# Performance work log

Measured on AMD Instinct MI355X. Metric: run time of the kernel, lower is better.

## Reference

```python
import jax, jax.numpy as jnp
import numpy as np

QUALITY = 8
N_PART = 18000 * QUALITY ** 2  # 1,152,000
N_GRID = 128 * QUALITY         # 1024
DX = 1.0 / N_GRID
INV_DX = float(N_GRID)
DT = 1e-4 / QUALITY
P_VOL = (DX * 0.5) ** 2
P_MASS = P_VOL * 1.0
E_MOD, NU = 5000.0, 0.2
MU0 = E_MOD / (2.0 * (1.0 + NU))
LAM0 = E_MOD * NU / ((1.0 + NU) * (1.0 - 2.0 * NU))
OFF = jnp.array([[i, j] for i in range(3) for j in range(3)], dtype=jnp.int32)  # [9,2]


def setup_inputs() -> dict:
    key = jax.random.key(0)
    ks = jax.random.split(key, 6)
    x = 0.05 + 0.9 * jax.random.uniform(ks[0], (N_PART, 2), dtype=jnp.float32)
    v = jax.random.normal(ks[1], (N_PART, 2), dtype=jnp.float32)
    C = 0.1 * jax.random.normal(ks[2], (N_PART, 2, 2), dtype=jnp.float32)
    F = jnp.eye(2, dtype=jnp.float32) + 0.02 * jax.random.normal(ks[3], (N_PART, 2, 2), dtype=jnp.float32)
    material = jax.random.randint(ks[4], (N_PART,), 0, 3, dtype=jnp.int32)
    Jp = 0.5 + jax.random.uniform(ks[5], (N_PART,), dtype=jnp.float32)
    gravity = jnp.array([0.0, -1.0], dtype=jnp.float32)
    attractor_strength = jnp.array(1.0, dtype=jnp.float32)
    attractor_pos = jnp.array([0.5, 0.5], dtype=jnp.float32)
    return dict(x=x, v=v, C=C, F=F, Jp=Jp, gravity=gravity,
                attractor_strength=attractor_strength, attractor_pos=attractor_pos,
                material=material)


def _substep(x, v, C, F, Jp, gravity, attractor_strength, attractor_pos, material):
    I2 = jnp.eye(2, dtype=x.dtype)
    # ---- per-particle quadratic B-spline weights ----
    base = jnp.floor(x * INV_DX - 0.5).astype(jnp.int32)            # [P,2]
    fx = x * INV_DX - base.astype(x.dtype)                           # [P,2]
    w = jnp.stack([0.5 * (1.5 - fx) ** 2,
                   0.75 - (fx - 1.0) ** 2,
                   0.5 * (fx - 0.5) ** 2], axis=1)                   # [P,3,2]
    weight = w[:, OFF[:, 0], 0] * w[:, OFF[:, 1], 1]                 # [P,9]

    # ---- deformation update + elastoplastic stress ----
    F = jnp.einsum('pij,pjk->pik', I2 + DT * C, F)                   # [P,2,2]
    h = jnp.clip(jnp.exp(10.0 * (1.0 - Jp)), 0.1, 5.0)
    h = jnp.where(material == 1, 0.3, h)
    mu = jnp.where(material == 0, 0.0, MU0 * h)                      # [P]
    la = LAM0 * h
    U, sig, Vh = jnp.linalg.svd(F)                                   # sig [P,2]
    new_sig = jnp.where((material == 2)[:, None],
                        jnp.clip(sig, 1.0 - 2.5e-2, 1.0 + 4.5e-3), sig)
    Jp = Jp * jnp.prod(sig / new_sig, axis=1)
    J = jnp.prod(new_sig, axis=1)                                    # [P]
    F_fluid = jnp.sqrt(J)[:, None, None] * I2
    F_snow = jnp.einsum('pij,pj,pjk->pik', U, new_sig, Vh)
    F = jnp.where((material == 0)[:, None, None], F_fluid,
                  jnp.where((material == 2)[:, None, None], F_snow, F))
    R = jnp.einsum('pij,pjk->pik', U, Vh)                            # rotation U V^T
    stress = (2.0 * mu[:, None, None] *
              jnp.einsum('pij,pkj->pik', F - R, F) +
              (la * J * (J - 1.0))[:, None, None] * I2)
    stress = (-DT * P_VOL * 4.0 * INV_DX * INV_DX) * stress
    affine = stress + P_MASS * C                                     # [P,2,2]

    # ---- P2G scatter-add ----
    dpos = (OFF.astype(x.dtype)[None] - fx[:, None, :]) * DX         # [P,9,2]
    mom = weight[:, :, None] * (P_MASS * v[:, None, :] +
                                jnp.einsum('pab,pkb->pka', affine, dpos))
    gi = jnp.clip(base[:, None, 0] + OFF[None, :, 0], 0, N_GRID - 1)
    gj = jnp.clip(base[:, None, 1] + OFF[None, :, 1], 0, N_GRID - 1)
    idx = (gi * N_GRID + gj).reshape(-1)                              # [P*9]
    grid_v = jnp.zeros((N_GRID * N_GRID, 2), x.dtype).at[idx].add(mom.reshape(-1, 2))
    grid_m = jnp.zeros((N_GRID * N_GRID,), x.dtype).at[idx].add((weight * P_MASS).reshape(-1))

    # ---- grid update ----
    gv = grid_v.reshape(N_GRID, N_GRID, 2)
    gm = grid_m.reshape(N_GRID, N_GRID)
    mask = gm > 0
    gv = jnp.where(mask[..., None], gv / jnp.where(mask, gm, 1.0)[..., None], 0.0)
    gv = gv + DT * 30.0 * gravity                                    # broadcast [2]
    ii, jj = jnp.meshgrid(jnp.arange(N_GRID), jnp.arange(N_GRID), indexing='ij')
    coords = DX * jnp.stack([ii, jj], axis=-1).astype(x.dtype)        # [G,G,2]
    dist = attractor_pos - coords
    gv = gv + dist / (0.01 + jnp.linalg.norm(dist, axis=-1, keepdims=True)) \
              * attractor_strength * DT * 100.0
    gvx, gvy = gv[..., 0], gv[..., 1]
    gvx = jnp.where((ii < 3) & (gvx < 0), 0.0, gvx)
    gvx = jnp.where((ii > N_GRID - 3) & (gvx > 0), 0.0, gvx)
    gvy = jnp.where((jj < 3) & (gvy < 0), 0.0, gvy)
    gvy = jnp.where((jj > N_GRID - 3) & (gvy > 0), 0.0, gvy)
    gv = jnp.where(mask[..., None], jnp.stack([gvx, gvy], axis=-1), 0.0)

    # ---- G2P gather ----
    g_v = gv.reshape(N_GRID * N_GRID, 2)[idx].reshape(-1, 9, 2)       # [P,9,2]
    new_v = jnp.einsum('pk,pka->pa', weight, g_v)
    dpos_g = OFF.astype(x.dtype)[None] - fx[:, None, :]               # unscaled
    new_C = 4.0 * INV_DX * jnp.einsum('pk,pka,pkb->pab', weight, g_v, dpos_g)
    x_new = x + DT * new_v
    return x_new, new_v, new_C, F, Jp


def reference(x, v, C, F, Jp, gravity, attractor_strength, attractor_pos, material):
    return _substep(x, v, C, F, Jp, gravity, attractor_strength, attractor_pos, material)
```

## Files before the change

### kernel.cpp

```cpp
#include <hip/hip_runtime.h>
#include <hip/hip_fp16.h>
#include <math.h>

namespace {
constexpr int   QUALITY = 8;
constexpr int   NPART   = 18000 * QUALITY * QUALITY;
constexpr int   NG      = 128 * QUALITY;
constexpr int   NCELL   = NG * NG;
constexpr int   CT      = 16;
constexpr int   NBT     = NG / CT;
constexpr float DX      = 1.0f / (float)NG;
constexpr float INV_DX  = (float)NG;
constexpr float DT      = (float)(1e-4 / (double)QUALITY);
constexpr float MU0     = (float)(5000.0 / (2.0 * (1.0 + 0.2)));
constexpr float LAM0    = (float)(5000.0 * 0.2 / ((1.0 + 0.2) * (1.0 - 0.4)));
constexpr float STRESS_RP  = (float)(-(1e-4 / 8.0) * 4.0 * 1024.0 * 1024.0);
constexpr float GRAV_SCALE = (float)((1e-4 / 8.0) * 30.0);
constexpr float ATTR_SCALE = (float)((1e-4 / 8.0) * 100.0);

typedef int v4i __attribute__((ext_vector_type(4)));

__device__ __forceinline__ int2 base_of(float xx, float xy) {
    int bx = (int)floorf(xx * INV_DX - 0.5f);
    int by = (int)floorf(xy * INV_DX - 0.5f);
    bx = min(max(bx, 0), NG - 3);
    by = min(max(by, 0), NG - 3);
    return make_int2(bx, by);
}

__device__ __forceinline__ unsigned pack2h(float a, float b) {
    __half2 h = __floats2half2_rn(a, b);
    return *reinterpret_cast<unsigned*>(&h);
}
__device__ __forceinline__ float2 unpack2h(unsigned u) {
    __half2 h = *reinterpret_cast<__half2*>(&u);
    return __half22float2(h);
}

__device__ __forceinline__ float bspline(float s) {
    s = fabsf(s);
    float a = 0.75f - s * s;
    float b = 1.5f - s;
    b = 0.5f * b * b;
    return (s < 0.5f) ? a : b;
}
}

__global__ __launch_bounds__(256)
void count_kernel(const float* __restrict__ x, int* __restrict__ cnt,
                  int* __restrict__ rank) {
    int p = blockIdx.x * blockDim.x + threadIdx.x;
    if (p >= NPART) return;
    const float2 xv = ((const float2*)x)[p];
    int2 b = base_of(xv.x, xv.y);
    rank[p] = atomicAdd(&cnt[b.x * NG + b.y], 1);
}

__global__ __launch_bounds__(256)
void blocksum_kernel(const int* __restrict__ cnt, int* __restrict__ bsum) {
    __shared__ int sh[256];
    int t = threadIdx.x;
    int4 c = ((const int4*)cnt)[blockIdx.x * 256 + t];
    sh[t] = c.x + c.y + c.z + c.w;
    __syncthreads();
    for (int s = 128; s > 0; s >>= 1) {
        if (t < s) sh[t] += sh[t + s];
        __syncthreads();
    }
    if (t == 0) bsum[blockIdx.x] = sh[0];
}

__global__ __launch_bounds__(1024)
void scanb_kernel(const int* __restrict__ bsum, int* __restrict__ boff,
                  int* __restrict__ cell_start) {
    __shared__ int s[1024];
    int t = threadIdx.x;
    int v = bsum[t];
    s[t] = v;
    __syncthreads();
    for (int off = 1; off < 1024; off <<= 1) {
        int add = (t >= off) ? s[t - off] : 0;
        __syncthreads();
        s[t] += add;
        __syncthreads();
    }
    boff[t] = s[t] - v;
    if (t == 1023) cell_start[NCELL] = s[t];
}

__global__ __launch_bounds__(256)
void scanc_kernel(const int* __restrict__ cnt, const int* __restrict__ boff,
                  int* __restrict__ cell_start) {
    __shared__ int tsum[256];
    int t = threadIdx.x;
    int gbase4 = blockIdx.x * 256 + t;
    int4 c = ((const int4*)cnt)[gbase4];
    int s1 = c.x, s2 = s1 + c.y, s3 = s2 + c.z, tot = s3 + c.w;
    tsum[t] = tot;
    __syncthreads();
    for (int off = 1; off < 256; off <<= 1) {
        int add = (t >= off) ? tsum[t - off] : 0;
        __syncthreads();
        tsum[t] += add;
        __syncthreads();
    }
    int excl = tsum[t] - tot;
    int g = boff[blockIdx.x] + excl;
    ((int4*)cell_start)[gbase4] = make_int4(g, g + s1, g + s2, g + s3);
}

__global__ __launch_bounds__(256)
void physics_scatter_kernel(const float* __restrict__ x, const float* __restrict__ v,
                            const float* __restrict__ Cin, const float* __restrict__ Fin,
                            const float* __restrict__ Jpin, const int* __restrict__ mat,
                            const int* __restrict__ cell_start, const int* __restrict__ rank,
                            uint4* __restrict__ spay,
                            float* __restrict__ outF, float* __restrict__ outJp)
{
    int p = blockIdx.x * blockDim.x + threadIdx.x;
    if (p >= NPART) return;

    const float2 xv = ((const float2*)x)[p];
    const float2 vv = ((const float2*)v)[p];
    const float4 Cv = ((const float4*)Cin)[p];
    const float4 Fv = ((const float4*)Fin)[p];
    float xx = xv.x, xy = xv.y;
    float C00 = Cv.x, C01 = Cv.y, C10 = Cv.z, C11 = Cv.w;
    float F00 = Fv.x, F01 = Fv.y, F10 = Fv.z, F11 = Fv.w;

    float A00 = 1.0f + DT * C00, A01 = DT * C01, A10 = DT * C10, A11 = 1.0f + DT * C11;
    float G00 = A00 * F00 + A01 * F10;
    float G01 = A00 * F01 + A01 * F11;
    float G10 = A10 * F00 + A11 * F10;
    float G11 = A10 * F01 + A11 * F11;

    int m = mat[p];
    float Jp = Jpin[p];
    float h = fminf(fmaxf(expf(10.0f * (1.0f - Jp)), 0.1f), 5.0f);
    if (m == 1) h = 0.3f;
    float mu = (m == 0) ? 0.0f : MU0 * h;
    float la = LAM0 * h;

    float Ee = 0.5f * (G00 + G11);
    float Hh = 0.5f * (G10 - G01);
    float Ff = 0.5f * (G00 - G11);
    float Gg = 0.5f * (G10 + G01);
    float Qq = sqrtf(Ee * Ee + Hh * Hh);
    float Rr = sqrtf(Ff * Ff + Gg * Gg);
    float s0 = Qq + Rr, s1 = Qq - Rr;
    float b1 = atan2f(Gg, Ff);
    float b2 = atan2f(Hh, Ee);
    float phi = 0.5f * (b1 + b2), th = 0.5f * (b1 - b2);
    float sphi, cphi, sth, cth;
    sincosf(phi, &sphi, &cphi);
    sincosf(th, &sth, &cth);

    float ns0 = s0, ns1 = s1;
    if (m == 2) {
        ns0 = fminf(fmaxf(s0, 1.0f - 2.5e-2f), 1.0f + 4.5e-3f);
        ns1 = fminf(fmaxf(s1, 1.0f - 2.5e-2f), 1.0f + 4.5e-3f);
        Jp = Jp * (s0 / ns0) * (s1 / ns1);
    }
    float J = ns0 * ns1;

    float FF00, FF01, FF10, FF11;
    if (m == 0) {
        float sj = sqrtf(J);
        FF00 = sj; FF01 = 0.0f; FF10 = 0.0f; FF11 = sj;
    } else if (m == 2) {
        FF00 = ns0 * cphi * cth + ns1 * sphi * sth;
        FF01 = ns0 * cphi * sth - ns1 * sphi * cth;
        FF10 = ns0 * sphi * cth - ns1 * cphi * sth;
        FF11 = ns0 * sphi * sth + ns1 * cphi * cth;
    } else {
        FF00 = G00; FF01 = G01; FF10 = G10; FF11 = G11;
    }

    float cr = cphi * cth + sphi * sth;
    float sr = sphi * cth - cphi * sth;

    float D00 = FF00 - cr,  D01 = FF01 + sr;
    float D10 = FF10 - sr,  D11 = FF11 - cr;
    float S00 = D00 * FF00 + D01 * FF01;
    float S01 = D00 * FF10 + D01 * FF11;
    float S10 = D10 * FF00 + D11 * FF01;
    float S11 = D10 * FF10 + D11 * FF11;
    float lj = la * J * (J - 1.0f);
    S00 = 2.0f * mu * S00 + lj;
    S01 = 2.0f * mu * S01;
    S10 = 2.0f * mu * S10;
    S11 = 2.0f * mu * S11 + lj;
    float a00 = STRESS_RP * S00 + C00;
    float a01 = STRESS_RP * S01 + C01;
    float a10 = STRESS_RP * S10 + C10;
    float a11 = STRESS_RP * S11 + C11;

    ((float4*)outF)[p] = make_float4(FF00, FF01, FF10, FF11);
    outJp[p] = Jp;

    float bxf = floorf(xx * INV_DX - 0.5f);
    float byf = floorf(xy * INV_DX - 0.5f);
    float fxx = xx * INV_DX - bxf;
    float fxy = xy * INV_DX - byf;
    unsigned qx = (unsigned)__float2int_rn((fxx - 0.5f) * 16383.0f);
    unsigned qy = (unsigned)__float2int_rn((fxy - 0.5f) * 16383.0f);

    int2 b = base_of(xx, xy);

    v4i payload;
    payload.x = (int)((qx & 0x3FFFu) | ((qy & 0x3FFFu) << 16) | (((unsigned)b.y & 3u) << 30));
    payload.y = (int)pack2h(vv.x, vv.y);
    payload.z = (int)pack2h(a00, a01);
    payload.w = (int)pack2h(a10, a11);

    int pos = cell_start[b.x * NG + b.y] + rank[p];
    __builtin_nontemporal_store(payload, (v4i*)&spay[pos]);
}

__global__ __launch_bounds__(256)
void p2g_gather_grid_kernel(const uint4* __restrict__ spay,
                            const int* __restrict__ cell_start,
                            const float* __restrict__ grav,
                            const float* __restrict__ astr,
                            const float* __restrict__ apos,
                            float* __restrict__ gv)
{
    int tile = blockIdx.x;
    int lr = threadIdx.x / CT;
    int lc = threadIdx.x % CT;
    int cx = (tile / NBT) * CT + lr;
    int cy = (tile % NBT) * CT + lc;

    float svx = 0.0f, svy = 0.0f, sw = 0.0f;
    int c0 = max(cy - 2, 0);
    float fcy = (float)cy;

    #pragma unroll
    for (int d = 0; d < 3; ++d) {
        int r = cx - 2 + d;
        if (r < 0 || r > NG - 1) continue;
        int row = r * NG;
        int s = cell_start[row + c0];
        int e = cell_start[row + cy + 1];
        const float io = (float)(2 - d);
        for (int t = s; t < e; ++t) {
            uint4 q = spay[t];
            float fxx = 0.5f + (float)(q.x & 0x3FFFu) * (1.0f / 16383.0f);
            float fxy = 0.5f + (float)((q.x >> 16) & 0x3FFFu) * (1.0f / 16383.0f);
            float fj = (float)((cy - (int)(q.x >> 30)) & 3);
            float wx;
            if (d == 0)      wx = 0.5f * (fxx - 0.5f) * (fxx - 0.5f);
            else if (d == 1) wx = 0.75f - (fxx - 1.0f) * (fxx - 1.0f);
            else             wx = 0.5f * (1.5f - fxx) * (1.5f - fxx);
            float wy = bspline(fxy - fj);
            float w = wx * wy;
            float2 vv = unpack2h(q.y);
            float2 aA = unpack2h(q.z);
            float2 aB = unpack2h(q.w);
            float dpx = (io - fxx) * DX;
            float dpy = (fj - fxy) * DX;
            svx += w * (vv.x + aA.x * dpx + aA.y * dpy);
            svy += w * (vv.y + aB.x * dpx + aB.y * dpy);
            sw  += w;
        }
    }

    float vx = 0.0f, vy = 0.0f;
    if (sw > 0.0f) {
        float inv = 1.0f / sw;
        vx = svx * inv + GRAV_SCALE * grav[0];
        vy = svy * inv + GRAV_SCALE * grav[1];
        float dxp = apos[0] - DX * (float)cx;
        float dyp = apos[1] - DX * fcy;
        float nrm = sqrtf(dxp * dxp + dyp * dyp);
        float k = astr[0] * ATTR_SCALE / (0.01f + nrm);
        vx += dxp * k;
        vy += dyp * k;
        if (cx < 3 && vx < 0.0f) vx = 0.0f;
        if (cx > NG - 3 && vx > 0.0f) vx = 0.0f;
        if (cy < 3 && vy < 0.0f) vy = 0.0f;
        if (cy > NG - 3 && vy > 0.0f) vy = 0.0f;
    }
    ((float2*)gv)[cx * NG + cy] = make_float2(vx, vy);
}

__global__ __launch_bounds__(256)
void g2p_kernel(const float* __restrict__ x, const float* __restrict__ gv,
                float* __restrict__ outX, float* __restrict__ outV,
                float* __restrict__ outC)
{
    int p = blockIdx.x * blockDim.x + threadIdx.x;
    if (p >= NPART) return;

    const float2 xv = ((const float2*)x)[p];
    float xx = xv.x, xy = xv.y;
    float bxf = floorf(xx * INV_DX - 0.5f);
    float byf = floorf(xy * INV_DX - 0.5f);
    int bx = (int)bxf, by = (int)byf;
    float fxx = xx * INV_DX - bxf;
    float fxy = xy * INV_DX - byf;

    float wxs[3], wys[3];
    wxs[0] = 0.5f * (1.5f - fxx) * (1.5f - fxx);
    wxs[1] = 0.75f - (fxx - 1.0f) * (fxx - 1.0f);
    wxs[2] = 0.5f * (fxx - 0.5f) * (fxx - 0.5f);
    wys[0] = 0.5f * (1.5f - fxy) * (1.5f - fxy);
    wys[1] = 0.75f - (fxy - 1.0f) * (fxy - 1.0f);
    wys[2] = 0.5f * (fxy - 0.5f) * (fxy - 0.5f);

    int a0 = min(max(by & ~1, 0), NG - 4);
    bool odd = (by - a0) == 1;

    float nvx = 0.0f, nvy = 0.0f;
    float c00 = 0.0f, c01 = 0.0f, c10 = 0.0f, c11 = 0.0f;

    #pragma unroll
    for (int i = 0; i < 3; ++i) {
        int gi = min(max(bx + i, 0), NG - 1);
        float dpx = (float)i - fxx;
        const float4* rowp = (const float4*)(gv + gi * NG * 2 + a0 * 2);
        float4 A = rowp[0];
        float4 B = rowp[1];
        float g0x = odd ? A.z : A.x,  g0y = odd ? A.w : A.y;
        float g1x = odd ? B.x : A.z,  g1y = odd ? B.y : A.w;
        float g2x = odd ? B.z : B.x,  g2y = odd ? B.w : B.y;
        float w0 = wxs[i] * wys[0];
        float w1 = wxs[i] * wys[1];
        float w2 = wxs[i] * wys[2];
        float dpy0 = 0.0f - fxy, dpy1 = 1.0f - fxy, dpy2 = 2.0f - fxy;
        nvx += w0 * g0x + w1 * g1x + w2 * g2x;
        nvy += w0 * g0y + w1 * g1y + w2 * g2y;
        c00 += dpx * (w0 * g0x + w1 * g1x + w2 * g2x);
        c01 += w0 * g0x * dpy0 + w1 * g1x * dpy1 + w2 * g2x * dpy2;
        c10 += dpx * (w0 * g0y + w1 * g1y + w2 * g2y);
        c11 += w0 * g0y * dpy0 + w1 * g1y * dpy1 + w2 * g2y * dpy2;
    }
    float cs = 4.0f * INV_DX;
    ((float2*)outV)[p] = make_float2(nvx, nvy);
    ((float2*)outX)[p] = make_float2(xx + DT * nvx, xy + DT * nvy);
    ((float4*)outC)[p] = make_float4(cs * c00, cs * c01, cs * c10, cs * c11);
}

extern "C" void kernel_launch(void* const* d_in, const int* in_sizes, int n_in,
                              void* d_out, int out_size, void* d_ws, size_t ws_size,
                              hipStream_t stream)
{
    const float* x    = (const float*)d_in[0];
    const float* v    = (const float*)d_in[1];
    const float* C    = (const float*)d_in[2];
    const float* F    = (const float*)d_in[3];
    const float* Jp   = (const float*)d_in[4];
    const float* grav = (const float*)d_in[5];
    const float* astr = (const float*)d_in[6];
    const float* apos = (const float*)d_in[7];
    const int*   mat  = (const int*)d_in[8];

    float* out   = (float*)d_out;
    float* outX  = out;
    float* outV  = out + 2 * NPART;
    float* outC  = out + 4 * NPART;
    float* outF  = out + 8 * NPART;
    float* outJp = out + 12 * NPART;

    int*   ws_i      = (int*)d_ws;
    int*   cnt       = ws_i;
    float* gv        = (float*)d_ws;
    int*   cell_start= ws_i + 2 * NCELL;
    int*   bsum      = cell_start + NCELL + 1;
    int*   boff      = bsum + 1024;
    int*   rank      = boff + 1024;
    size_t off       = (size_t)(3 * NCELL + 2 * 1024 + 1 + NPART);
    off = (off + 3) & ~(size_t)3;
    uint4* spay      = (uint4*)(ws_i + off);

    const int TB = 256;
    hipMemsetAsync(cnt, 0, (size_t)NCELL * sizeof(int), stream);
    count_kernel   <<<(NPART + TB - 1) / TB, TB, 0, stream>>>(x, cnt, rank);
    blocksum_kernel<<<NCELL / 1024, TB, 0, stream>>>(cnt, bsum);
    scanb_kernel   <<<1, 1024, 0, stream>>>(bsum, boff, cell_start);
    scanc_kernel   <<<NCELL / 1024, TB, 0, stream>>>(cnt, boff, cell_start);
    physics_scatter_kernel<<<(NPART + TB - 1) / TB, TB, 0, stream>>>(
        x, v, C, F, Jp, mat, cell_start, rank, spay, outF, outJp);
    p2g_gather_grid_kernel<<<NBT * NBT, TB, 0, stream>>>(
        spay, cell_start, grav, astr, apos, gv);
    g2p_kernel     <<<(NPART + TB - 1) / TB, TB, 0, stream>>>(x, gv, outX, outV, outC);
}
```

Measured before the change: 181.4 us.

## Stage tile halo particles in shared memory for P2G grid gather

The P2G gather kernel now loads each 16x16 tile's 18x18 halo of particles once from global memory, decodes them into shared memory with tile-relative positions, and each grid cell then reads its 3x3 neighborhood from LDS instead of re-reading and re-decoding global payloads up to nine times. A fallback keeps the old global path when a tile holds more than 768 particles. This costs about 27KB of LDS per block, which lowers occupancy, and adds serial prefix work on one thread.

```diff
diff --git a/kernel.cpp b/kernel.cpp
--- a/kernel.cpp
+++ b/kernel.cpp
@@ -9,6 +9,9 @@
 constexpr int   NCELL   = NG * NG;
 constexpr int   CT      = 16;
 constexpr int   NBT     = NG / CT;
+constexpr int   WROWS   = 18;
+constexpr int   WCOLS   = 18;
+constexpr int   CAP     = 768;
 constexpr float DX      = 1.0f / (float)NG;
 constexpr float INV_DX  = (float)NG;
 constexpr float DT      = (float)(1e-4 / (double)QUALITY);
@@ -218,50 +221,130 @@
 }
 
 __global__ __launch_bounds__(256)
-void p2g_gather_grid_kernel(const uint4* __restrict__ spay,
-                            const int* __restrict__ cell_start,
-                            const float* __restrict__ grav,
-                            const float* __restrict__ astr,
-                            const float* __restrict__ apos,
-                            float* __restrict__ gv)
+void p2g_tile_kernel(const uint4* __restrict__ spay,
+                     const int* __restrict__ cell_start,
+                     const float* __restrict__ grav,
+                     const float* __restrict__ astr,
+                     const float* __restrict__ apos,
+                     float* __restrict__ gv)
 {
+    __shared__ int   csA[WROWS * (WCOLS + 1)];
+    __shared__ int   offl[WROWS * (WCOLS + 1)];
+    __shared__ int   rowbase[WROWS];
+    __shared__ int   s_total;
+    __shared__ float part[CAP * 8];
+
     int tile = blockIdx.x;
-    int lr = threadIdx.x / CT;
-    int lc = threadIdx.x % CT;
-    int cx = (tile / NBT) * CT + lr;
-    int cy = (tile % NBT) * CT + lc;
-
+    int x0 = (tile / NBT) * CT;
+    int y0 = (tile % NBT) * CT;
+    int tid = threadIdx.x;
+
+    for (int i = tid; i < WROWS * (WCOLS + 1); i += 256) {
+        int wr = i / (WCOLS + 1), wc = i % (WCOLS + 1);
+        int gr = x0 - 2 + wr;
+        int c  = y0 - 2 + wc;
+        int val = 0;
+        if (gr >= 0 && gr < NG) {
+            int cc = min(max(c, 0), NG);
+            val = cell_start[gr * NG + cc];
+        }
+        csA[i] = val;
+    }
+    __syncthreads();
+
+    if (tid == 0) {
+        int base = 0;
+        for (int wr = 0; wr < WROWS; ++wr) {
+            rowbase[wr] = base;
+            base += csA[wr * (WCOLS + 1) + WCOLS] - csA[wr * (WCOLS + 1)];
+        }
+        s_total = base;
+    }
+    __syncthreads();
+    int total = s_total;
+    bool staged = (total <= CAP);
+
+    if (staged) {
+        for (int i = tid; i < WROWS * (WCOLS + 1); i += 256) {
+            int wr = i / (WCOLS + 1);
+            offl[i] = rowbase[wr] + csA[i] - csA[wr * (WCOLS + 1)];
+        }
+        __syncthreads();
+        for (int ci = tid; ci < WROWS * WCOLS; ci += 256) {
+            int wr = ci / WCOLS, wc = ci % WCOLS;
+            int sbeg = csA[wr * (WCOLS + 1) + wc];
+            int send = csA[wr * (WCOLS + 1) + wc + 1];
+            int slot = offl[wr * (WCOLS + 1) + wc];
+            float frow = (float)wr, fcol = (float)wc;
+            for (int t = sbeg; t < send; ++t, ++slot) {
+                uint4 q = spay[t];
+                float fx_rel = frow + 0.5f + (float)(q.x & 0x3FFFu) * (1.0f / 16383.0f);
+                float fy_rel = fcol + 0.5f + (float)((q.x >> 16) & 0x3FFFu) * (1.0f / 16383.0f);
+                float2 vv = unpack2h(q.y);
+                float2 aA = unpack2h(q.z);
+                float2 aB = unpack2h(q.w);
+                float* pp = &part[slot * 8];
+                ((float4*)pp)[0] = make_float4(fx_rel, fy_rel, vv.x, vv.y);
+                ((float4*)pp)[1] = make_float4(aA.x, aA.y, aB.x, aB.y);
+            }
+        }
+    }
+    __syncthreads();
+
+    int tr = tid / CT, tc = tid % CT;
+    int cx = x0 + tr, cy = y0 + tc;
     float svx = 0.0f, svy = 0.0f, sw = 0.0f;
-    int c0 = max(cy - 2, 0);
-    float fcy = (float)cy;
-
-    #pragma unroll
-    for (int d = 0; d < 3; ++d) {
-        int r = cx - 2 + d;
-        if (r < 0 || r > NG - 1) continue;
-        int row = r * NG;
-        int s = cell_start[row + c0];
-        int e = cell_start[row + cy + 1];
-        const float io = (float)(2 - d);
-        for (int t = s; t < e; ++t) {
-            uint4 q = spay[t];
-            float fxx = 0.5f + (float)(q.x & 0x3FFFu) * (1.0f / 16383.0f);
-            float fxy = 0.5f + (float)((q.x >> 16) & 0x3FFFu) * (1.0f / 16383.0f);
-            float fj = (float)((cy - (int)(q.x >> 30)) & 3);
-            float wx;
-            if (d == 0)      wx = 0.5f * (fxx - 0.5f) * (fxx - 0.5f);
-            else if (d == 1) wx = 0.75f - (fxx - 1.0f) * (fxx - 1.0f);
-            else             wx = 0.5f * (1.5f - fxx) * (1.5f - fxx);
-            float wy = bspline(fxy - fj);
-            float w = wx * wy;
-            float2 vv = unpack2h(q.y);
-            float2 aA = unpack2h(q.z);
-            float2 aB = unpack2h(q.w);
-            float dpx = (io - fxx) * DX;
-            float dpy = (fj - fxy) * DX;
-            svx += w * (vv.x + aA.x * dpx + aA.y * dpy);
-            svy += w * (vv.y + aB.x * dpx + aB.y * dpy);
-            sw  += w;
+
+    if (staged) {
+        float cxw = (float)(tr + 2);
+        float cyw = (float)(tc + 2);
+        #pragma unroll
+        for (int d = 0; d < 3; ++d) {
+            int wr = tr + d;
+            int sbeg = offl[wr * (WCOLS + 1) + tc];
+            int send = offl[wr * (WCOLS + 1) + tc + 3];
+            for (int s = sbeg; s < send; ++s) {
+                const float* pp = &part[s * 8];
+                float4 P0 = ((const float4*)pp)[0];
+                float4 P1 = ((const float4*)pp)[1];
+                float w = bspline(P0.x - cxw) * bspline(P0.y - cyw);
+                float dpx = (cxw - P0.x) * DX;
+                float dpy = (cyw - P0.y) * DX;
+                svx += w * (P0.z + P1.x * dpx + P1.y * dpy);
+                svy += w * (P0.w + P1.z * dpx + P1.w * dpy);
+                sw  += w;
+            }
+        }
+    } else {
+        int c0 = max(cy - 2, 0);
+        #pragma unroll
+        for (int d = 0; d < 3; ++d) {
+            int r = cx - 2 + d;
+            if (r < 0 || r > NG - 1) continue;
+            int row = r * NG;
+            int s = cell_start[row + c0];
+            int e = cell_start[row + cy + 1];
+            const float io = (float)(2 - d);
+            for (int t = s; t < e; ++t) {
+                uint4 q = spay[t];
+                float fxx = 0.5f + (float)(q.x & 0x3FFFu) * (1.0f / 16383.0f);
+                float fxy = 0.5f + (float)((q.x >> 16) & 0x3FFFu) * (1.0f / 16383.0f);
+                float fj = (float)((cy - (int)(q.x >> 30)) & 3);
+                float wx;
+                if (d == 0)      wx = 0.5f * (fxx - 0.5f) * (fxx - 0.5f);
+                else if (d == 1) wx = 0.75f - (fxx - 1.0f) * (fxx - 1.0f);
+                else             wx = 0.5f * (1.5f - fxx) * (1.5f - fxx);
+                float wy = bspline(fxy - fj);
+                float w = wx * wy;
+                float2 vv = unpack2h(q.y);
+                float2 aA = unpack2h(q.z);
+                float2 aB = unpack2h(q.w);
+                float dpx = (io - fxx) * DX;
+                float dpy = (fj - fxy) * DX;
+                svx += w * (vv.x + aA.x * dpx + aA.y * dpy);
+                svy += w * (vv.y + aB.x * dpx + aB.y * dpy);
+                sw  += w;
+            }
         }
     }
 
@@ -271,7 +354,7 @@
         vx = svx * inv + GRAV_SCALE * grav[0];
         vy = svy * inv + GRAV_SCALE * grav[1];
         float dxp = apos[0] - DX * (float)cx;
-        float dyp = apos[1] - DX * fcy;
+        float dyp = apos[1] - DX * (float)cy;
         float nrm = sqrtf(dxp * dxp + dyp * dyp);
         float k = astr[0] * ATTR_SCALE / (0.01f + nrm);
         vx += dxp * k;
@@ -381,7 +464,7 @@
     scanc_kernel   <<<NCELL / 1024, TB, 0, stream>>>(cnt, boff, cell_start);
     physics_scatter_kernel<<<(NPART + TB - 1) / TB, TB, 0, stream>>>(
         x, v, C, F, Jp, mat, cell_start, rank, spay, outF, outJp);
-    p2g_gather_grid_kernel<<<NBT * NBT, TB, 0, stream>>>(
+    p2g_tile_kernel<<<NBT * NBT, TB, 0, stream>>>(
         spay, cell_start, grav, astr, apos, gv);
     g2p_kernel     <<<(NPART + TB - 1) / TB, TB, 0, stream>>>(x, gv, outX, outV, outC);
 }
```

New measurement: 185.2 us. 2.1% more time.
